# Performance work log

Hardware: AMD Instinct MI355X
Metric: run time of the kernel (lower is better)

Reference implementation:

```python
import jax, jax.numpy as jnp
import numpy as np

N_TYPES = 10
BATCH = 16
SEQ = 512
STEPS = 10          # quadrature steps per interval (original hard-codes 10)
T_HORIZON = 100.0   # observation window end
T_MAX_EVENT = 90.0  # events strictly inside [0, T)


def setup_inputs() -> dict:
    key = jax.random.key(0)
    k1, k2, k3, k4, k5 = jax.random.split(key, 5)
    # sorted positive event times so the `times >= 0` filter in the original is a no-op
    event_times = jnp.sort(
        jax.random.uniform(k1, (BATCH, SEQ), dtype=jnp.float32) * T_MAX_EVENT, axis=1)
    event_types = jax.random.randint(k2, (BATCH, SEQ), 0, N_TYPES)
    # parameters, initialized exactly like _initialize_parameters()
    mu = jax.random.uniform(k3, (N_TYPES,), minval=0.01, maxval=0.1, dtype=jnp.float32)
    alpha = jax.random.uniform(k4, (N_TYPES, N_TYPES), minval=0.01, maxval=0.1, dtype=jnp.float32)
    beta = jax.random.uniform(k5, (N_TYPES, N_TYPES), minval=0.5, maxval=1.5, dtype=jnp.float32)
    T = jnp.asarray(T_HORIZON, dtype=jnp.float32)
    return {"event_times": event_times, "event_types": event_types, "T": T,
            "mu": mu, "alpha": alpha, "beta": beta}


def _hawkes_nll(event_times, event_types, T, mu, alpha, beta):
    B, S = event_times.shape
    dtype = event_times.dtype

    # ---- term 1: sum_i lambda_{type_i}(t_i | history) (original sums the raw
    # intensity, NOT its log -- reproduced faithfully) ----
    tj = event_types[:, None, :]            # past event type  (j axis)
    ti = event_types[:, :, None]            # current event type (i axis)
    dt = event_times[:, :, None] - event_times[:, None, :]   # [B, i, j] = t_i - t_j
    causal = jnp.arange(S)[:, None] > jnp.arange(S)[None, :]  # j < i
    dt_safe = jnp.where(causal[None], dt, 0.0)
    A = alpha[tj, ti]                        # alpha[type_j, type_i]  [B, S, S]
    Bm = beta[tj, ti]
    infl = jnp.where(causal[None], A * jnp.exp(-Bm * dt_safe), 0.0).sum(-1)  # [B, S]
    log_likelihood = (mu[event_types] + infl).sum()

    # ---- term 2: quadrature integral of total intensity over [0, T] ----
    # intervals: [0, t_1], [t_1, t_2], ..., [t_S, T]  -> S+1 intervals
    starts = jnp.concatenate([jnp.zeros((B, 1), dtype), event_times], axis=1)  # [B, S+1]
    ends = jnp.concatenate([event_times, jnp.broadcast_to(T, (B, 1)).astype(dtype)], axis=1)
    h = (ends - starts) / STEPS                                               # [B, S+1]
    # history for interval i is {j : t_j <= start_i} = {j < i} (sorted distinct times)
    hist = jnp.arange(S + 1)[:, None] > jnp.arange(S)[None, :]                # [S+1, S]
    arow = alpha[event_types]                # alpha[type_j, :]  [B, S, K]
    brow = beta[event_types]                 # beta[type_j, :]   [B, S, K]

    acc = jnp.zeros((B, S + 1), dtype)       # sum over quadrature points of influence
    for p in range(STEPS + 1):
        tp = starts + p * h                                                   # [B, S+1]
        dtp = jnp.where(hist[None], tp[:, :, None] - event_times[:, None, :], 0.0)  # [B,S+1,S]
        dec = jnp.exp(-brow[:, None] * dtp[..., None])                        # [B,S+1,S,K]
        acc = acc + jnp.where(hist[None, :, :, None], arow[:, None] * dec, 0.0).sum((2, 3))
    # each of the STEPS+1 quadrature points also contributes mu.sum()
    vals = acc + (STEPS + 1) * mu.sum()
    integral = (vals * h).sum()

    return -(log_likelihood - integral)


def reference(event_times, event_types, T, mu, alpha, beta):
    return _hawkes_nll(event_times, event_types, T, mu, alpha, beta)
```

## Files before the change

### kernel.cpp

```cpp
#include <hip/hip_runtime.h>

#define NT      10
#define NBATCH  16
#define SEQ     512
#define KSTEPS  10
#define NC      16
#define CL      (SEQ / NC)
#define SPLIT   5
#define SPB     (NT * NT / SPLIT)
#define THREADS (NC * SPB)
#define NBLOCKS (NBATCH * SPLIT)


__global__ __launch_bounds__(THREADS) void hawkes_fused(
    const float* __restrict__ times, const int* __restrict__ types,
    const float* __restrict__ Tptr,  const float* __restrict__ mu,
    const float* __restrict__ alpha, const float* __restrict__ beta,
    float* __restrict__ partial)
{
    __shared__ float s_time[SEQ];
    __shared__ int   s_ty[SEQ];
    __shared__ float cA[NC][SPB], cB[NC][SPB], cC[NC][SPB],
                     cD[NC][SPB], cE[NC][SPB], cF[NC][SPB];
    __shared__ float s_part[SPB];

    const int blk = blockIdx.x;
    const int b   = blk / SPLIT;
    const int sp  = blk - b * SPLIT;
    const int t   = threadIdx.x;

    const float* bt  = times + b * SEQ;
    const int*   bty = types + b * SEQ;
    #pragma unroll
    for (int i = t; i < SEQ; i += THREADS) { s_time[i] = bt[i]; s_ty[i] = bty[i]; }
    __syncthreads();

    const int c  = t / SPB;
    const int sl = t - c * SPB;
    const int s  = sp * SPB + sl;
    const int a  = s / NT;
    const int m  = s - a * NT;
    const float al  = alpha[a * NT + m];
    const float be  = beta [a * NT + m];
    const float mum = (a == 0) ? mu[m] : 0.f;

    float A = 1.f, gl = 0.f, C_ = 0.f, D = 0.f, E = 0.f, F = 0.f;
    const int k0 = c * CL;
    float tprev = (c == 0) ? 0.f : s_time[k0 - 1];

    #pragma unroll 8
    for (int i = 0; i < CL; ++i) {
        const float te   = s_time[k0 + i];
        const float h    = (te - tprev) * (1.0f / KSTEPS);
        tprev = te;
        const float x    = be * h;
        const float e1   = __expf(-x);
        const float e10  = __expf(-10.f * x);
        const float gA   = (1.f - e10 * e1) * __builtin_amdgcn_rcpf(1.f - e1);
        const float gB   = 11.f + x * (-55.f + 192.5f * x);
        const float geom = (x > 1e-3f) ? gA : gB;
        const float coef = al * geom * h;
        C_ = fmaf(coef, A,  C_);
        D  = fmaf(coef, gl, D);
        A  *= e10;
        gl *= e10;
        const int ty = s_ty[k0 + i];
        E  = (ty == m) ? fmaf(al, A,  E) : E;
        F  = (ty == m) ? (F + fmaf(al, gl, mum)) : F;
        gl += (ty == a) ? 1.f : 0.f;
    }
    if (c == NC - 1) {
        const float h    = (Tptr[0] - tprev) * (1.0f / KSTEPS);
        const float x    = be * h;
        const float e1   = __expf(-x);
        const float e10  = __expf(-10.f * x);
        const float gA   = (1.f - e10 * e1) * __builtin_amdgcn_rcpf(1.f - e1);
        const float gB   = 11.f + x * (-55.f + 192.5f * x);
        const float geom = (x > 1e-3f) ? gA : gB;
        const float coef = al * geom * h;
        C_ = fmaf(coef, A,  C_);
        D  = fmaf(coef, gl, D);
    }

    cA[c][sl] = A;  cB[c][sl] = gl;
    cC[c][sl] = C_; cD[c][sl] = D;
    cE[c][sl] = E;  cF[c][sl] = F;
    __syncthreads();

    if (t < SPB) {
        float g = 0.f, I = 0.f, Lk = 0.f;
        #pragma unroll
        for (int cc = 0; cc < NC; ++cc) {
            I  += fmaf(cC[cc][t], g, cD[cc][t]);
            Lk += fmaf(cE[cc][t], g, cF[cc][t]);
            g   = fmaf(cA[cc][t], g, cB[cc][t]);
        }
        s_part[t] = I - Lk;
    }
    __syncthreads();
    if (t == 0) {
        float S = 0.f;
        #pragma unroll
        for (int i = 0; i < SPB; ++i) S += s_part[i];
        partial[blk] = S;
    }
}

__global__ __launch_bounds__(128) void hawkes_sum(
    const float* __restrict__ partial, const float* __restrict__ mu,
    const float* __restrict__ Tptr, float* __restrict__ out)
{
    const int t = threadIdx.x;
    float S = (t < NBLOCKS) ? partial[t] : 0.f;
    for (int off = 32; off; off >>= 1) S += __shfl_down(S, off);
    __shared__ float red[2];
    if ((t & 63) == 0) red[t >> 6] = S;
    __syncthreads();
    if (t == 0) {
        float mus = 0.f;
        #pragma unroll
        for (int i = 0; i < NT; ++i) mus += mu[i];
        const float cst = (float)NBATCH * (float)(KSTEPS + 1) * mus * Tptr[0] * (1.0f / KSTEPS);
        out[0] = red[0] + red[1] + cst;
    }
}

extern "C" void kernel_launch(void* const* d_in, const int* in_sizes, int n_in,
                              void* d_out, int out_size, void* d_ws, size_t ws_size,
                              hipStream_t stream) {
    const float* times = (const float*)d_in[0];
    const int*   types = (const int*)d_in[1];
    const float* T     = (const float*)d_in[2];
    const float* mu    = (const float*)d_in[3];
    const float* alpha = (const float*)d_in[4];
    const float* beta  = (const float*)d_in[5];
    float* partial = (float*)d_ws;
    float* out     = (float*)d_out;

    hawkes_fused<<<NBLOCKS, THREADS, 0, stream>>>(times, types, T, mu, alpha, beta, partial);
    hawkes_sum<<<1, 128, 0, stream>>>(partial, mu, T, out);
}
```

Measured before the change: 12.59 us.

## Restructure Hawkes scan into single-wavefront blocks with shuffle-based chunk combine

Each 64-thread block now handles two (a,m) type pairs for one batch, with 32 chunks of 16 events per pair. Every lane loads its chunk with vectorized float4/int4 global loads instead of staging through shared memory. The serial 16-chunk shared-memory combine becomes a log-depth associative shuffle scan over the six linear-recurrence coefficients. This removes the __syncthreads barriers and the serial combine tail and raises the block count to 800. In exchange it adds more shuffle work and a larger partial array for the final reduction kernel to sum.

```diff
diff --git a/kernel.cpp b/kernel.cpp
--- a/kernel.cpp
+++ b/kernel.cpp
@@ -1,58 +1,73 @@
 #include <hip/hip_runtime.h>
 
-#define NT      10
-#define NBATCH  16
-#define SEQ     512
-#define KSTEPS  10
-#define NC      16
-#define CL      (SEQ / NC)
-#define SPLIT   5
-#define SPB     (NT * NT / SPLIT)
-#define THREADS (NC * SPB)
-#define NBLOCKS (NBATCH * SPLIT)
+#define NT    10
+#define NB    16
+#define SEQ   512
+#define KST   10
+#define NCH   32
+#define CLEN  (SEQ / NCH)
+#define GRP   50
+#define NBLK  (NB * GRP)
 
 
-__global__ __launch_bounds__(THREADS) void hawkes_fused(
+__global__ __launch_bounds__(64) void hawkes_scan(
     const float* __restrict__ times, const int* __restrict__ types,
     const float* __restrict__ Tptr,  const float* __restrict__ mu,
     const float* __restrict__ alpha, const float* __restrict__ beta,
     float* __restrict__ partial)
 {
-    __shared__ float s_time[SEQ];
-    __shared__ int   s_ty[SEQ];
-    __shared__ float cA[NC][SPB], cB[NC][SPB], cC[NC][SPB],
-                     cD[NC][SPB], cE[NC][SPB], cF[NC][SPB];
-    __shared__ float s_part[SPB];
+    const int blk  = blockIdx.x;
+    const int b    = blk / GRP;
+    const int grp  = blk - b * GRP;
+    const int lane = threadIdx.x;
+    const int half = lane >> 5;
+    const int c    = lane & 31;
+    const int s    = grp * 2 + half;
+    const int a    = s / NT;
+    const int m    = s - a * NT;
 
-    const int blk = blockIdx.x;
-    const int b   = blk / SPLIT;
-    const int sp  = blk - b * SPLIT;
-    const int t   = threadIdx.x;
-
-    const float* bt  = times + b * SEQ;
-    const int*   bty = types + b * SEQ;
-    #pragma unroll
-    for (int i = t; i < SEQ; i += THREADS) { s_time[i] = bt[i]; s_ty[i] = bty[i]; }
-    __syncthreads();
-
-    const int c  = t / SPB;
-    const int sl = t - c * SPB;
-    const int s  = sp * SPB + sl;
-    const int a  = s / NT;
-    const int m  = s - a * NT;
     const float al  = alpha[a * NT + m];
     const float be  = beta [a * NT + m];
     const float mum = (a == 0) ? mu[m] : 0.f;
 
-    float A = 1.f, gl = 0.f, C_ = 0.f, D = 0.f, E = 0.f, F = 0.f;
-    const int k0 = c * CL;
-    float tprev = (c == 0) ? 0.f : s_time[k0 - 1];
+    const float4* tp = (const float4*)(times + b * SEQ + c * CLEN);
+    const int4*   yp = (const int4*)  (types + b * SEQ + c * CLEN);
+    const float4 T0 = tp[0], T1 = tp[1], T2 = tp[2], T3 = tp[3];
+    const int4   Y0 = yp[0], Y1 = yp[1], Y2 = yp[2], Y3 = yp[3];
 
-    #pragma unroll 8
-    for (int i = 0; i < CL; ++i) {
-        const float te   = s_time[k0 + i];
-        const float h    = (te - tprev) * (1.0f / KSTEPS);
-        tprev = te;
+    float tprev = __shfl(T3.w, lane - 1, 64);
+    if (c == 0) tprev = 0.f;
+
+    float A = 1.f, B = 0.f, C = 0.f, D = 0.f, E = 0.f, F = 0.f;
+
+#define STEP(TE, TY)                                                          \
+    {                                                                         \
+        const float h    = ((TE) - tprev) * (1.0f / KST);                     \
+        tprev = (TE);                                                         \
+        const float x    = be * h;                                            \
+        const float e1   = __expf(-x);                                        \
+        const float e10  = __expf(-10.f * x);                                 \
+        const float gA   = (1.f - e10 * e1) * __builtin_amdgcn_rcpf(1.f - e1);\
+        const float gB   = 11.f + x * (-55.f + 192.5f * x);                   \
+        const float geom = (x > 1e-3f) ? gA : gB;                             \
+        const float coef = al * geom * h;                                     \
+        C = fmaf(coef, A, C);                                                 \
+        D = fmaf(coef, B, D);                                                 \
+        A *= e10;                                                             \
+        B *= e10;                                                             \
+        E = ((TY) == m) ? fmaf(al, A, E) : E;                                 \
+        F = ((TY) == m) ? (F + fmaf(al, B, mum)) : F;                         \
+        B += ((TY) == a) ? 1.f : 0.f;                                         \
+    }
+
+    STEP(T0.x, Y0.x) STEP(T0.y, Y0.y) STEP(T0.z, Y0.z) STEP(T0.w, Y0.w)
+    STEP(T1.x, Y1.x) STEP(T1.y, Y1.y) STEP(T1.z, Y1.z) STEP(T1.w, Y1.w)
+    STEP(T2.x, Y2.x) STEP(T2.y, Y2.y) STEP(T2.z, Y2.z) STEP(T2.w, Y2.w)
+    STEP(T3.x, Y3.x) STEP(T3.y, Y3.y) STEP(T3.z, Y3.z) STEP(T3.w, Y3.w)
+#undef STEP
+
+    if (c == NCH - 1) {
+        const float h    = (Tptr[0] - tprev) * (1.0f / KST);
         const float x    = be * h;
         const float e1   = __expf(-x);
         const float e10  = __expf(-10.f * x);
@@ -60,68 +75,53 @@
         const float gB   = 11.f + x * (-55.f + 192.5f * x);
         const float geom = (x > 1e-3f) ? gA : gB;
         const float coef = al * geom * h;
-        C_ = fmaf(coef, A,  C_);
-        D  = fmaf(coef, gl, D);
-        A  *= e10;
-        gl *= e10;
-        const int ty = s_ty[k0 + i];
-        E  = (ty == m) ? fmaf(al, A,  E) : E;
-        F  = (ty == m) ? (F + fmaf(al, gl, mum)) : F;
-        gl += (ty == a) ? 1.f : 0.f;
-    }
-    if (c == NC - 1) {
-        const float h    = (Tptr[0] - tprev) * (1.0f / KSTEPS);
-        const float x    = be * h;
-        const float e1   = __expf(-x);
-        const float e10  = __expf(-10.f * x);
-        const float gA   = (1.f - e10 * e1) * __builtin_amdgcn_rcpf(1.f - e1);
-        const float gB   = 11.f + x * (-55.f + 192.5f * x);
-        const float geom = (x > 1e-3f) ? gA : gB;
-        const float coef = al * geom * h;
-        C_ = fmaf(coef, A,  C_);
-        D  = fmaf(coef, gl, D);
+        C = fmaf(coef, A, C);
+        D = fmaf(coef, B, D);
     }
 
-    cA[c][sl] = A;  cB[c][sl] = gl;
-    cC[c][sl] = C_; cD[c][sl] = D;
-    cE[c][sl] = E;  cF[c][sl] = F;
-    __syncthreads();
+    #pragma unroll
+    for (int msk = 1; msk < 32; msk <<= 1) {
+        const float pA = __shfl_xor(A, msk, 32);
+        const float pB = __shfl_xor(B, msk, 32);
+        const float pC = __shfl_xor(C, msk, 32);
+        const float pD = __shfl_xor(D, msk, 32);
+        const float pE = __shfl_xor(E, msk, 32);
+        const float pF = __shfl_xor(F, msk, 32);
+        const bool e = ((lane & msk) == 0);
+        const float Af = e ? A : pA, Bf = e ? B : pB, Cf = e ? C : pC,
+                    Df = e ? D : pD, Ef = e ? E : pE, Ff = e ? F : pF;
+        const float Ag = e ? pA : A, Bg = e ? pB : B, Cg = e ? pC : C,
+                    Dg = e ? pD : D, Eg = e ? pE : E, Fg = e ? pF : F;
+        A = Ag * Af;
+        B = fmaf(Ag, Bf, Bg);
+        C = fmaf(Cg, Af, Cf);
+        D = Df + fmaf(Cg, Bf, Dg);
+        E = fmaf(Eg, Af, Ef);
+        F = Ff + fmaf(Eg, Bf, Fg);
+    }
 
-    if (t < SPB) {
-        float g = 0.f, I = 0.f, Lk = 0.f;
-        #pragma unroll
-        for (int cc = 0; cc < NC; ++cc) {
-            I  += fmaf(cC[cc][t], g, cD[cc][t]);
-            Lk += fmaf(cE[cc][t], g, cF[cc][t]);
-            g   = fmaf(cA[cc][t], g, cB[cc][t]);
-        }
-        s_part[t] = I - Lk;
-    }
-    __syncthreads();
-    if (t == 0) {
-        float S = 0.f;
-        #pragma unroll
-        for (int i = 0; i < SPB; ++i) S += s_part[i];
-        partial[blk] = S;
-    }
+    const float v  = D - F;
+    const float v2 = __shfl(v, lane ^ 32, 64);
+    if (lane == 0) partial[blk] = v + v2;
 }
 
-__global__ __launch_bounds__(128) void hawkes_sum(
+__global__ __launch_bounds__(256) void hawkes_sum(
     const float* __restrict__ partial, const float* __restrict__ mu,
     const float* __restrict__ Tptr, float* __restrict__ out)
 {
     const int t = threadIdx.x;
-    float S = (t < NBLOCKS) ? partial[t] : 0.f;
-    for (int off = 32; off; off >>= 1) S += __shfl_down(S, off);
-    __shared__ float red[2];
+    float S = 0.f;
+    for (int i = t; i < NBLK; i += 256) S += partial[i];
+    for (int off = 32; off; off >>= 1) S += __shfl_down(S, off, 64);
+    __shared__ float red[4];
     if ((t & 63) == 0) red[t >> 6] = S;
     __syncthreads();
     if (t == 0) {
         float mus = 0.f;
         #pragma unroll
         for (int i = 0; i < NT; ++i) mus += mu[i];
-        const float cst = (float)NBATCH * (float)(KSTEPS + 1) * mus * Tptr[0] * (1.0f / KSTEPS);
-        out[0] = red[0] + red[1] + cst;
+        const float cst = (float)NB * (float)(KST + 1) * mus * Tptr[0] * (1.0f / KST);
+        out[0] = red[0] + red[1] + red[2] + red[3] + cst;
     }
 }
 
@@ -137,6 +137,6 @@
     float* partial = (float*)d_ws;
     float* out     = (float*)d_out;
 
-    hawkes_fused<<<NBLOCKS, THREADS, 0, stream>>>(times, types, T, mu, alpha, beta, partial);
-    hawkes_sum<<<1, 128, 0, stream>>>(partial, mu, T, out);
+    hawkes_scan<<<NBLK, 64, 0, stream>>>(times, types, T, mu, alpha, beta, partial);
+    hawkes_sum<<<1, 256, 0, stream>>>(partial, mu, T, out);
 }
```

Result: faster. 11.45 us (median of 2 runs) (-9.1%).
